# Kernel optimization log

Hardware: AMD Instinct MI355X
Metric: run time of the kernel (lower is better)

## Reference

```python
import jax, jax.numpy as jnp
import numpy as np

GRID = 14
N_HEADS = 12
TOP_K = 32


def _valid_indices(grid):
    """Replicates create_locality_mask: cls row/col always valid; patch pairs
    valid iff Chebyshev distance on the grid <= 2 (includes diagonal)."""
    n = grid * grid + 1
    mask = np.zeros((n, n), dtype=bool)
    mask[0, :] = True
    mask[:, 0] = True
    idx = np.arange(grid * grid)
    r, c = idx // grid, idx % grid
    cheb = np.maximum(np.abs(r[:, None] - r[None, :]), np.abs(c[:, None] - c[None, :]))
    mask[1:, 1:] = cheb <= 2
    i_idx, j_idx = np.nonzero(mask)
    return jnp.asarray(i_idx, dtype=jnp.int32), jnp.asarray(j_idx, dtype=jnp.int32)

I_IDX, J_IDX = _valid_indices(GRID)  # nv = 4489 valid (query, key) pairs


def setup_inputs() -> dict:
    key = jax.random.key(0)
    ks = jax.random.split(key, 6)
    B, L, D = 32, GRID * GRID + 1, 768
    s = 0.02
    return {
        "x": jax.random.normal(ks[0], (B, L, D), jnp.float32),
        "W_q": jax.random.normal(ks[1], (D, D), jnp.float32) * s,
        "b_q": jnp.zeros((D,), jnp.float32),
        "W_k": jax.random.normal(ks[2], (D, D), jnp.float32) * s,
        "b_k": jnp.zeros((D,), jnp.float32),
        "W_v": jax.random.normal(ks[3], (D, D), jnp.float32) * s,
        "b_v": jnp.zeros((D,), jnp.float32),
        "W_o": jax.random.normal(ks[4], (D, D), jnp.float32) * s,
        "b_o": jnp.zeros((D,), jnp.float32),
        "log_sigma": jnp.zeros((), jnp.float32),  # sigma = 1.0
    }


def reference(x, W_q, b_q, W_k, b_k, W_v, b_v, W_o, b_o, log_sigma):
    B, L, D = x.shape
    H, dk = N_HEADS, D // N_HEADS

    def proj(W, b):
        y = jnp.einsum('bld,de->ble', x, W) + b
        return y.reshape(B, L, H, dk).transpose(0, 2, 1, 3)  # [B,H,L,dk]

    Q, K, V = proj(W_q, b_q), proj(W_k, b_k), proj(W_v, b_v)

    sigma_sq = jnp.exp(2.0 * log_sigma)
    # gather valid (i,j) pairs; nv pairs from the locality mask
    q_valid = Q[:, :, I_IDX, :]                       # [B,H,nv,dk]
    k_valid = K[:, :, J_IDX, :]                       # [B,H,nv,dk]
    dist_sq = jnp.sum((q_valid - k_valid) ** 2, axis=-1)  # [B,H,nv]
    scores_valid = (-0.5 / sigma_sq) * dist_sq

    neg_inf = jnp.array(-jnp.inf, x.dtype)
    scores = jnp.full((B, H, L, L), neg_inf, dtype=x.dtype)
    scores = scores.at[:, :, I_IDX, J_IDX].set(scores_valid)

    k_top = min(TOP_K, L)
    _, top_idx = jax.lax.top_k(scores, k_top)          # [B,H,L,k]
    bb = jnp.arange(B)[:, None, None, None]
    hh = jnp.arange(H)[None, :, None, None]
    nn = jnp.arange(L)[None, None, :, None]
    topk_mask = jnp.zeros((B, H, L, L), bool).at[bb, hh, nn, top_idx].set(True)

    final_mask = jnp.isfinite(scores) & topk_mask
    scores = jnp.where(final_mask, scores, neg_inf)
    weights = jax.nn.softmax(scores, axis=-1)          # [B,H,L,L]
    attention_mask = (weights > 1e-6).astype(x.dtype)

    consensus = jnp.einsum('bhij,bhjd->bhid', weights, V)
    consensus = consensus.transpose(0, 2, 1, 3).reshape(B, L, D)
    out = jnp.einsum('bld,de->ble', consensus, W_o) + b_o
    return out, weights, attention_mask
```

## Files before the change

kernel.cpp:

```cpp
#include <hip/hip_runtime.h>
#include <hip/hip_bf16.h>
#include <math.h>

#define GRIDN 14
#define L 197
#define H 12
#define DK 64
#define D 768
#define B 32
#define BL (B*L)
#define TOPK 32
#define NBH (B*H)
#define NROW (NBH*L)
#define QKV_ELEMS ((size_t)NROW*DK)

typedef __attribute__((ext_vector_type(8))) short short8;
typedef __attribute__((ext_vector_type(4))) float floatx4;

__device__ __forceinline__ void load_lds16(void* lds, const void* g) {
    __builtin_amdgcn_global_load_lds(
        (const __attribute__((address_space(1))) unsigned int*)g,
        (__attribute__((address_space(3))) unsigned int*)lds, 16, 0, 0);
}

__global__ __launch_bounds__(256)
void prep(const float* __restrict__ x,
          const float* __restrict__ Wq, const float* __restrict__ Wk,
          const float* __restrict__ Wv, const float* __restrict__ Wo,
          __hip_bfloat16* __restrict__ xh, __hip_bfloat16* __restrict__ xl,
          __hip_bfloat16* __restrict__ WqTh, __hip_bfloat16* __restrict__ WqTl,
          __hip_bfloat16* __restrict__ WkTh, __hip_bfloat16* __restrict__ WkTl,
          __hip_bfloat16* __restrict__ WvT,  __hip_bfloat16* __restrict__ WoT)
{
    const int z = blockIdx.z;
    if (z == 4) {
        int lin = (blockIdx.y * 24 + blockIdx.x) * 256 + threadIdx.x;
        for (int i = lin; i < BL * D / 4; i += 24 * 24 * 256) {
            float4 v = ((const float4*)x)[i];
            union { __hip_bfloat16 b[4]; short4 s; } hh, ll;
            float f[4] = {v.x, v.y, v.z, v.w};
            #pragma unroll
            for (int j = 0; j < 4; ++j) {
                __hip_bfloat16 h = __float2bfloat16(f[j]);
                hh.b[j] = h;
                ll.b[j] = __float2bfloat16(f[j] - __bfloat162float(h));
            }
            ((short4*)xh)[i] = hh.s;
            ((short4*)xl)[i] = ll.s;
        }
        return;
    }
    __shared__ float tile[32][33];
    const float* src = (z == 0) ? Wq : (z == 1) ? Wk : (z == 2) ? Wv : Wo;
    __hip_bfloat16* dh = (z == 0) ? WqTh : (z == 1) ? WkTh : (z == 2) ? WvT : WoT;
    __hip_bfloat16* dl = (z == 0) ? WqTl : (z == 1) ? WkTl : nullptr;
    const int k0 = blockIdx.y * 32, n0 = blockIdx.x * 32;
    const int tx = threadIdx.x & 31, ty = threadIdx.x >> 5;

    for (int r = ty; r < 32; r += 8)
        tile[r][tx] = src[(size_t)(k0 + r) * D + n0 + tx];
    __syncthreads();
    for (int r = ty; r < 32; r += 8) {
        float v = tile[tx][r];
        __hip_bfloat16 h = __float2bfloat16(v);
        dh[(size_t)(n0 + r) * D + k0 + tx] = h;
        if (dl) dl[(size_t)(n0 + r) * D + k0 + tx] =
            __float2bfloat16(v - __bfloat162float(h));
    }
}

__global__ __launch_bounds__(256)
void gemm_qkv(const __hip_bfloat16* __restrict__ xh, const __hip_bfloat16* __restrict__ xl,
              const __hip_bfloat16* __restrict__ Wqh, const __hip_bfloat16* __restrict__ Wql,
              const __hip_bfloat16* __restrict__ Wkh, const __hip_bfloat16* __restrict__ Wkl,
              const __hip_bfloat16* __restrict__ Wvh,
              const float* __restrict__ bq, const float* __restrict__ bk,
              const float* __restrict__ bv,
              float* __restrict__ Qb, float* __restrict__ Kb, float* __restrict__ Vb)
{
    __shared__ __attribute__((aligned(16))) __hip_bfloat16 Ash[128 * 32];
    __shared__ __attribute__((aligned(16))) __hip_bfloat16 Bsh[128 * 32];
    __shared__ __attribute__((aligned(16))) __hip_bfloat16 Asl[128 * 32];
    __shared__ __attribute__((aligned(16))) __hip_bfloat16 Bsl[128 * 32];

    const int grp = blockIdx.y / 6, nt = blockIdx.y % 6;
    const __hip_bfloat16 *Bth, *Btl; const float* bias; float* C;
    if (grp == 0)      { Bth = Wqh; Btl = Wql; bias = bq; C = Qb; }
    else if (grp == 1) { Bth = Wkh; Btl = Wkl; bias = bk; C = Kb; }
    else               { Bth = Wvh; Btl = nullptr; bias = bv; C = Vb; }
    const bool split = (grp < 2);

    const int tid = threadIdx.x;
    const int wave = tid >> 6, lane = tid & 63;
    const int quad = lane >> 4, l16 = lane & 15;
    const int m0 = blockIdx.x * 128, n0 = nt * 128;
    const int wm = (wave & 1) * 64, wn = (wave >> 1) * 64;

    floatx4 acc[4][4] = {};

    int s_r[2], s_cs[2];
    #pragma unroll
    for (int u = 0; u < 2; ++u) {
        int idx = tid + u * 256;
        s_r[u] = idx >> 2; s_cs[u] = idx & 3;
    }

    for (int k0 = 0; k0 < D; k0 += 32) {
        #pragma unroll
        for (int u = 0; u < 2; ++u) {
            int r = s_r[u];
            int csrc = s_cs[u] ^ ((r >> 1) & 3);
            int gm = m0 + r; if (gm >= BL) gm = BL - 1;
            size_t aoff = (size_t)gm * D + k0 + csrc * 8;
            size_t boff = (size_t)(n0 + r) * D + k0 + csrc * 8;
            int lds_off = (wave * 64 + u * 256) * 16;
            load_lds16((char*)Ash + lds_off, xh + aoff);
            load_lds16((char*)Bsh + lds_off, Bth + boff);
            if (split) {
                load_lds16((char*)Asl + lds_off, xl + aoff);
                load_lds16((char*)Bsl + lds_off, Btl + boff);
            }
        }
        __syncthreads();

        short8 ah[4], bh[4];
        #pragma unroll
        for (int a = 0; a < 4; ++a) {
            int r = wm + a * 16 + l16;
            int slot = (r << 2) + (quad ^ ((r >> 1) & 3));
            ah[a] = *(const short8*)((const char*)Ash + (slot << 4));
        }
        #pragma unroll
        for (int b2 = 0; b2 < 4; ++b2) {
            int r = wn + b2 * 16 + l16;
            int slot = (r << 2) + (quad ^ ((r >> 1) & 3));
            bh[b2] = *(const short8*)((const char*)Bsh + (slot << 4));
        }
        if (split) {
            short8 al[4], bl[4];
            #pragma unroll
            for (int a = 0; a < 4; ++a) {
                int r = wm + a * 16 + l16;
                int slot = (r << 2) + (quad ^ ((r >> 1) & 3));
                al[a] = *(const short8*)((const char*)Asl + (slot << 4));
            }
            #pragma unroll
            for (int b2 = 0; b2 < 4; ++b2) {
                int r = wn + b2 * 16 + l16;
                int slot = (r << 2) + (quad ^ ((r >> 1) & 3));
                bl[b2] = *(const short8*)((const char*)Bsl + (slot << 4));
            }
            #pragma unroll
            for (int a = 0; a < 4; ++a)
                #pragma unroll
                for (int b2 = 0; b2 < 4; ++b2) {
                    acc[a][b2] = __builtin_amdgcn_mfma_f32_16x16x32_bf16(
                        al[a], bh[b2], acc[a][b2], 0, 0, 0);
                    acc[a][b2] = __builtin_amdgcn_mfma_f32_16x16x32_bf16(
                        ah[a], bl[b2], acc[a][b2], 0, 0, 0);
                }
        }
        #pragma unroll
        for (int a = 0; a < 4; ++a)
            #pragma unroll
            for (int b2 = 0; b2 < 4; ++b2)
                acc[a][b2] = __builtin_amdgcn_mfma_f32_16x16x32_bf16(
                    ah[a], bh[b2], acc[a][b2], 0, 0, 0);
        __syncthreads();
    }

    #pragma unroll
    for (int b2 = 0; b2 < 4; ++b2) {
        int n = n0 + wn + b2 * 16 + l16;
        float bvv = bias[n];
        int hh = n >> 6, dd = n & 63;
        #pragma unroll
        for (int a = 0; a < 4; ++a) {
            #pragma unroll
            for (int r = 0; r < 4; ++r) {
                int m = m0 + wm + a * 16 + quad * 4 + r;
                if (m < BL) {
                    int bb = m / L, ll = m % L;
                    C[((((size_t)bb * H + hh) * L + ll) << 6) + dd] =
                        acc[a][b2][r] + bvv;
                }
            }
        }
    }
}

__global__ __launch_bounds__(256)
void gemm_o(const __hip_bfloat16* __restrict__ A,
            const __hip_bfloat16* __restrict__ Bt,
            const float* __restrict__ bias, float* __restrict__ C)
{
    __shared__ __attribute__((aligned(16))) __hip_bfloat16 As[128 * 32];
    __shared__ __attribute__((aligned(16))) __hip_bfloat16 Bts[128 * 32];

    const int tid = threadIdx.x;
    const int wave = tid >> 6, lane = tid & 63;
    const int quad = lane >> 4, l16 = lane & 15;
    const int m0 = blockIdx.x * 128, n0 = blockIdx.y * 128;
    const int wm = (wave & 1) * 64, wn = (wave >> 1) * 64;

    floatx4 acc[4][4] = {};

    int s_r[2], s_cs[2];
    #pragma unroll
    for (int u = 0; u < 2; ++u) {
        int idx = tid + u * 256;
        s_r[u] = idx >> 2; s_cs[u] = idx & 3;
    }

    for (int k0 = 0; k0 < D; k0 += 32) {
        #pragma unroll
        for (int u = 0; u < 2; ++u) {
            int r = s_r[u];
            int csrc = s_cs[u] ^ ((r >> 1) & 3);
            int gm = m0 + r; if (gm >= BL) gm = BL - 1;
            int lds_off = (wave * 64 + u * 256) * 16;
            load_lds16((char*)As + lds_off, A + (size_t)gm * D + k0 + csrc * 8);
            load_lds16((char*)Bts + lds_off, Bt + (size_t)(n0 + r) * D + k0 + csrc * 8);
        }
        __syncthreads();

        short8 af[4], bf[4];
        #pragma unroll
        for (int a = 0; a < 4; ++a) {
            int r = wm + a * 16 + l16;
            int slot = (r << 2) + (quad ^ ((r >> 1) & 3));
            af[a] = *(const short8*)((const char*)As + (slot << 4));
        }
        #pragma unroll
        for (int b2 = 0; b2 < 4; ++b2) {
            int r = wn + b2 * 16 + l16;
            int slot = (r << 2) + (quad ^ ((r >> 1) & 3));
            bf[b2] = *(const short8*)((const char*)Bts + (slot << 4));
        }
        #pragma unroll
        for (int a = 0; a < 4; ++a)
            #pragma unroll
            for (int b2 = 0; b2 < 4; ++b2)
                acc[a][b2] = __builtin_amdgcn_mfma_f32_16x16x32_bf16(
                    af[a], bf[b2], acc[a][b2], 0, 0, 0);
        __syncthreads();
    }

    #pragma unroll
    for (int b2 = 0; b2 < 4; ++b2) {
        int n = n0 + wn + b2 * 16 + l16;
        float bvv = bias[n];
        #pragma unroll
        for (int a = 0; a < 4; ++a) {
            #pragma unroll
            for (int r = 0; r < 4; ++r) {
                int m = m0 + wm + a * 16 + quad * 4 + r;
                if (m < BL) C[(size_t)m * D + n] = acc[a][b2][r] + bvv;
            }
        }
    }
}

__global__ __launch_bounds__(512)
void attn_fused(const float* __restrict__ Q, const float* __restrict__ Kg,
                const float* __restrict__ Vg, const float* __restrict__ logsig,
                float* __restrict__ wout, float* __restrict__ mout,
                __hip_bfloat16* __restrict__ cons)
{
    __shared__ float qbuf[8][64];
    __shared__ float clsbuf[L];
    __shared__ float wjW[99][32];
    __shared__ unsigned char wjJ[99][32];
    __shared__ unsigned int winA[L];
    __shared__ unsigned int winB[L];
    __shared__ unsigned char joff[76];

    const int bh = blockIdx.x;
    const int yb = blockIdx.y;
    const int b = bh / H, h = bh % H;
    const int tid = threadIdx.x, wave = tid >> 6, lane = tid & 63;
    const int base_i = yb * 99;
    const int half = lane & 1;

    if (tid >= 1 && tid < L) {
        int r = (tid - 1) / GRIDN, c = (tid - 1) % GRIDN;
        int r0 = r - 2 < 0 ? 0 : r - 2, r1 = r + 2 > 13 ? 13 : r + 2;
        int c0 = c - 2 < 0 ? 0 : c - 2, c1 = c + 2 > 13 ? 13 : c + 2;
        int Wd = c1 - c0 + 1, Hh = r1 - r0 + 1;
        winA[tid] = (unsigned)r0 | ((unsigned)c0 << 8) |
                    ((unsigned)Wd << 16) | ((unsigned)Hh << 24);
        winB[tid] = (unsigned)(Hh * Wd + 1) |
                    ((unsigned)(1 + r0 * GRIDN + c0) << 8);
    }
    if (tid == 0) { winA[0] = 0; winB[0] = 0; }
    if (tid < 75) {
        int w = tid / 25 + 3, tm = tid % 25;
        joff[tid] = (unsigned char)((tm / w) * GRIDN + tm % w);
    }

    int pr4[4], pc4[4];
    #pragma unroll
    for (int k = 0; k < 4; ++k) {
        int p = lane + (k << 6);
        if (p >= 1 && p < L) { pr4[k] = (p - 1) / GRIDN; pc4[k] = (p - 1) % GRIDN; }
        else                 { pr4[k] = 255; pc4[k] = 255; }
    }

    const float* Kp = Kg + (size_t)bh * L * DK;
    const float* Vp = Vg + (size_t)bh * L * DK;
    __syncthreads();

    const float coef = -0.5f * expf(-2.0f * logsig[0]);
    const int starts0[9] = {0, 9, 22, 35, 48, 61, 74, 87, 99};
    const int starts1[9] = {99, 112, 124, 136, 148, 161, 173, 185, 197};
    const int i_begin = yb ? starts1[wave] : starts0[wave];
    const int i_end   = yb ? starts1[wave + 1] : starts0[wave + 1];

    float qreg = (i_begin < i_end)
               ? Q[((size_t)bh * L + i_begin) * 64 + lane] : 0.f;

    for (int i = i_begin; i < i_end; ++i) {
        const int rowid = bh * L + i;
        const size_t wb = (size_t)rowid * L;
        const int local = i - base_i;

        qbuf[wave][lane] = qreg;
        if (i + 1 < i_end)
            qreg = Q[((size_t)rowid + 1) * 64 + lane];

        if (i == 0) {
            const float4* qp = (const float4*)&qbuf[wave][half << 5];
            for (int p = 0; p < 7; ++p) {
                int t = (p << 5) + (lane >> 1);
                bool valid = t < L;
                float s = 0.f;
                if (valid) {
                    const float4* kp = (const float4*)&Kp[(size_t)t * DK + (half << 5)];
                    #pragma unroll
                    for (int d4 = 0; d4 < 8; ++d4) {
                        float4 qv = qp[d4], kv = kp[d4];
                        float dx = qv.x - kv.x, dy = qv.y - kv.y;
                        float dz = qv.z - kv.z, dw = qv.w - kv.w;
                        s += dx * dx + dy * dy + dz * dz + dw * dw;
                    }
                }
                s += __shfl_xor(s, 1);
                if (valid && !half) clsbuf[t] = coef * s;
            }
            float orig[4], cur[4]; int selb = 0;
            #pragma unroll
            for (int k = 0; k < 4; ++k) {
                int t = lane + (k << 6);
                float v = (t < L) ? clsbuf[t] : -INFINITY;
                orig[k] = v; cur[k] = v;
            }
            float gmax = -INFINITY;
            for (int it = 0; it < TOPK; ++it) {
                float bv = cur[0]; int bt = lane;
                #pragma unroll
                for (int k = 1; k < 4; ++k)
                    if (cur[k] > bv) { bv = cur[k]; bt = lane + (k << 6); }
                #pragma unroll
                for (int off = 32; off; off >>= 1) {
                    float ov = __shfl_xor(bv, off);
                    int   ot = __shfl_xor(bt, off);
                    if (ov > bv || (ov == bv && ot < bt)) { bv = ov; bt = ot; }
                }
                if (it == 0) gmax = bv;
                if ((bt & 63) == lane) { cur[bt >> 6] = -INFINITY; selb |= 1 << (bt >> 6); }
            }
            float zl = 0.f; float wk[4];
            #pragma unroll
            for (int k = 0; k < 4; ++k) {
                wk[k] = ((selb >> k) & 1) ? expf(orig[k] - gmax) : 0.f;
                zl += wk[k];
            }
            #pragma unroll
            for (int off = 32; off; off >>= 1) zl += __shfl_xor(zl, off);

            #pragma unroll
            for (int k = 0; k < 4; ++k) {
                int p = lane + (k << 6);
                if (p < L) {
                    float wv = wk[k] / zl;
                    wout[wb + p] = wv;
                    mout[wb + p] = (wv > 1e-6f) ? 1.f : 0.f;
                }
            }
            int slot = 0;
            #pragma unroll
            for (int k = 0; k < 4; ++k) {
                bool sel = (selb >> k) & 1;
                unsigned long long mk = __ballot(sel);
                if (sel) {
                    int tt = slot + (int)__popcll(mk & ((1ull << lane) - 1ull));
                    wjW[0][tt] = wk[k] / zl;
                    wjJ[0][tt] = (unsigned char)(lane + (k << 6));
                }
                slot += (int)__popcll(mk);
            }
        } else {
            const unsigned wa = winA[i], wbp = winB[i];
            const int r0 = wa & 255, c0 = (wa >> 8) & 255;
            const int Wd2 = (wa >> 16) & 255, Hh = wa >> 24;
            const int n = wbp & 255, jbase = wbp >> 8;

            int t = lane >> 1;
            bool valid = t < n;
            float s = 0.f; int j = 0;
            if (valid) {
                if (t > 0) j = jbase + joff[(Wd2 - 3) * 25 + (t - 1)];
                const float4* kp = (const float4*)&Kp[(size_t)j * DK + (half << 5)];
                const float4* qp = (const float4*)&qbuf[wave][half << 5];
                #pragma unroll
                for (int d4 = 0; d4 < 8; ++d4) {
                    float4 qv = qp[d4], kv = kp[d4];
                    float dx = qv.x - kv.x, dy = qv.y - kv.y;
                    float dz = qv.z - kv.z, dw = qv.w - kv.w;
                    s += dx * dx + dy * dy + dz * dz + dw * dw;
                }
            }
            s += __shfl_xor(s, 1);
            float sc = valid ? coef * s : -INFINITY;

            float mx = sc;
            #pragma unroll
            for (int off = 32; off; off >>= 1) mx = fmaxf(mx, __shfl_xor(mx, off));
            float e = valid ? expf(sc - mx) : 0.f;
            float es = half ? 0.f : e;
            #pragma unroll
            for (int off = 32; off; off >>= 1) es += __shfl_xor(es, off);
            float wv = e / es;

            if (!half) {
                float wcv = valid ? wv : 0.f;
                wjW[local][t] = wcv;
                wjJ[local][t] = (unsigned char)(valid ? j : 0);
            }
            #pragma unroll
            for (int k = 0; k < 4; ++k) {
                int p = lane + (k << 6);
                if (p < L) {
                    float wd = 0.f;
                    if (p == 0) wd = wjW[local][0];
                    else {
                        unsigned du = (unsigned)(pr4[k] - r0);
                        unsigned dv = (unsigned)(pc4[k] - c0);
                        if (du < (unsigned)Hh && dv < (unsigned)Wd2)
                            wd = wjW[local][1 + du * Wd2 + dv];
                    }
                    wout[wb + p] = wd;
                    mout[wb + p] = (wd > 1e-6f) ? 1.f : 0.f;
                }
            }
        }
    }
    __syncthreads();

    const int cstarts0[9] = {0, 13, 26, 38, 50, 62, 74, 87, 99};
    const int c_begin = yb ? starts1[wave] : cstarts0[wave];
    const int c_end   = yb ? starts1[wave + 1] : cstarts0[wave + 1];

    for (int i = c_begin; i < c_end; ++i) {
        const int local = i - base_i;
        float acc = 0.f;
        #pragma unroll
        for (int t = 0; t < 32; ++t) {
            float w = wjW[local][t];
            int j = wjJ[local][t];
            acc += w * Vp[(size_t)j * DK + lane];
        }
        cons[((size_t)b * L + i) * D + h * 64 + lane] = __float2bfloat16(acc);
    }
}

extern "C" void kernel_launch(void* const* d_in, const int* in_sizes, int n_in,
                              void* d_out, int out_size, void* d_ws, size_t ws_size,
                              hipStream_t stream)
{
    const float* x   = (const float*)d_in[0];
    const float* Wq  = (const float*)d_in[1];
    const float* bq  = (const float*)d_in[2];
    const float* Wk  = (const float*)d_in[3];
    const float* bk  = (const float*)d_in[4];
    const float* Wv  = (const float*)d_in[5];
    const float* bv  = (const float*)d_in[6];
    const float* Wo  = (const float*)d_in[7];
    const float* bo  = (const float*)d_in[8];
    const float* lsg = (const float*)d_in[9];

    float* out  = (float*)d_out;
    float* wout = out + QKV_ELEMS;
    float* mout = wout + (size_t)B * H * L * L;

    float* Qb  = (float*)d_ws;
    float* Kb  = Qb + QKV_ELEMS;
    float* Vb  = Kb + QKV_ELEMS;
    __hip_bfloat16* xh = (__hip_bfloat16*)(Vb + QKV_ELEMS);
    __hip_bfloat16* xl = xh + (size_t)BL * D;
    __hip_bfloat16* WqTh = xl + (size_t)BL * D;
    __hip_bfloat16* WqTl = WqTh + (size_t)D * D;
    __hip_bfloat16* WkTh = WqTl + (size_t)D * D;
    __hip_bfloat16* WkTl = WkTh + (size_t)D * D;
    __hip_bfloat16* WvT  = WkTl + (size_t)D * D;
    __hip_bfloat16* WoT  = WvT  + (size_t)D * D;
    __hip_bfloat16* consb = xh;

    prep<<<dim3(24, 24, 5), 256, 0, stream>>>(
        x, Wq, Wk, Wv, Wo, xh, xl, WqTh, WqTl, WkTh, WkTl, WvT, WoT);

    gemm_qkv<<<dim3(50, 18), 256, 0, stream>>>(
        xh, xl, WqTh, WqTl, WkTh, WkTl, WvT, bq, bk, bv, Qb, Kb, Vb);

    attn_fused<<<dim3(NBH, 2), 512, 0, stream>>>(
        Qb, Kb, Vb, lsg, wout, mout, consb);

    gemm_o<<<dim3(50, 6), 256, 0, stream>>>(consb, WoT, bo, out);
}
```

Measured before the change: 398.4 us.

## Stage K and V row windows in LDS for attention distance and consensus

Each attention block first copies the 127 K rows its half of the queries can touch (the cls row plus an offset window) into padded shared memory and computes distances from LDS rather than global memory. After the score phase, the same buffer is refilled with V rows for the weighted-sum step; the cls query row still reads V from global memory. Per-row window parameters are now computed arithmetically instead of through LDS lookup tables, and launch bounds request higher occupancy. This trades roughly 34KB of LDS and two extra barriers per block for fewer scattered global loads, which may reduce resident blocks per CU.

```diff
diff --git a/kernel.cpp b/kernel.cpp
--- a/kernel.cpp
+++ b/kernel.cpp
@@ -13,6 +13,8 @@
 #define NBH (B*H)
 #define NROW (NBH*L)
 #define QKV_ELEMS ((size_t)NROW*DK)
+#define KSTR 68
+#define KROWS 127
 
 typedef __attribute__((ext_vector_type(8))) short short8;
 typedef __attribute__((ext_vector_type(4))) float floatx4;
@@ -261,18 +263,17 @@
     }
 }
 
-__global__ __launch_bounds__(512)
+__global__ __launch_bounds__(512, 8)
 void attn_fused(const float* __restrict__ Q, const float* __restrict__ Kg,
                 const float* __restrict__ Vg, const float* __restrict__ logsig,
                 float* __restrict__ wout, float* __restrict__ mout,
                 __hip_bfloat16* __restrict__ cons)
 {
+    __shared__ __attribute__((aligned(16))) float KV[KROWS * KSTR];
     __shared__ float qbuf[8][64];
     __shared__ float clsbuf[L];
     __shared__ float wjW[99][32];
     __shared__ unsigned char wjJ[99][32];
-    __shared__ unsigned int winA[L];
-    __shared__ unsigned int winB[L];
     __shared__ unsigned char joff[76];
 
     const int bh = blockIdx.x;
@@ -281,18 +282,8 @@
     const int tid = threadIdx.x, wave = tid >> 6, lane = tid & 63;
     const int base_i = yb * 99;
     const int half = lane & 1;
-
-    if (tid >= 1 && tid < L) {
-        int r = (tid - 1) / GRIDN, c = (tid - 1) % GRIDN;
-        int r0 = r - 2 < 0 ? 0 : r - 2, r1 = r + 2 > 13 ? 13 : r + 2;
-        int c0 = c - 2 < 0 ? 0 : c - 2, c1 = c + 2 > 13 ? 13 : c + 2;
-        int Wd = c1 - c0 + 1, Hh = r1 - r0 + 1;
-        winA[tid] = (unsigned)r0 | ((unsigned)c0 << 8) |
-                    ((unsigned)Wd << 16) | ((unsigned)Hh << 24);
-        winB[tid] = (unsigned)(Hh * Wd + 1) |
-                    ((unsigned)(1 + r0 * GRIDN + c0) << 8);
-    }
-    if (tid == 0) { winA[0] = 0; winB[0] = 0; }
+    const int joffs = yb ? 70 : 0;
+
     if (tid < 75) {
         int w = tid / 25 + 3, tm = tid % 25;
         joff[tid] = (unsigned char)((tm / w) * GRIDN + tm % w);
@@ -307,7 +298,11 @@
     }
 
     const float* Kp = Kg + (size_t)bh * L * DK;
-    const float* Vp = Vg + (size_t)bh * L * DK;
+    for (int idx = tid; idx < KROWS * 16; idx += 512) {
+        int r = idx >> 4, c4 = idx & 15;
+        int g = r ? r + joffs : 0;
+        *(float4*)&KV[r * KSTR + c4 * 4] = *(const float4*)&Kp[g * 64 + c4 * 4];
+    }
     __syncthreads();
 
     const float coef = -0.5f * expf(-2.0f * logsig[0]);
@@ -400,17 +395,24 @@
                 slot += (int)__popcll(mk);
             }
         } else {
-            const unsigned wa = winA[i], wbp = winB[i];
-            const int r0 = wa & 255, c0 = (wa >> 8) & 255;
-            const int Wd2 = (wa >> 16) & 255, Hh = wa >> 24;
-            const int n = wbp & 255, jbase = wbp >> 8;
+            const int pi = i - 1;
+            const int pr = (pi * 9363) >> 17;
+            const int pc = pi - pr * GRIDN;
+            const int r0 = pr - 2 < 0 ? 0 : pr - 2;
+            const int r1 = pr + 2 > 13 ? 13 : pr + 2;
+            const int c0 = pc - 2 < 0 ? 0 : pc - 2;
+            const int c1 = pc + 2 > 13 ? 13 : pc + 2;
+            const int Wd2 = c1 - c0 + 1, Hh = r1 - r0 + 1;
+            const int n = Hh * Wd2 + 1;
+            const int jbase = 1 + r0 * GRIDN + c0;
 
             int t = lane >> 1;
             bool valid = t < n;
             float s = 0.f; int j = 0;
             if (valid) {
                 if (t > 0) j = jbase + joff[(Wd2 - 3) * 25 + (t - 1)];
-                const float4* kp = (const float4*)&Kp[(size_t)j * DK + (half << 5)];
+                int js = j ? j - joffs : 0;
+                const float4* kp = (const float4*)&KV[js * KSTR + (half << 5)];
                 const float4* qp = (const float4*)&qbuf[wave][half << 5];
                 #pragma unroll
                 for (int d4 = 0; d4 < 8; ++d4) {
@@ -457,6 +459,14 @@
     }
     __syncthreads();
 
+    const float* Vp = Vg + (size_t)bh * L * DK;
+    for (int idx = tid; idx < KROWS * 16; idx += 512) {
+        int r = idx >> 4, c4 = idx & 15;
+        int g = r ? r + joffs : 0;
+        *(float4*)&KV[r * KSTR + c4 * 4] = *(const float4*)&Vp[g * 64 + c4 * 4];
+    }
+    __syncthreads();
+
     const int cstarts0[9] = {0, 13, 26, 38, 50, 62, 74, 87, 99};
     const int c_begin = yb ? starts1[wave] : cstarts0[wave];
     const int c_end   = yb ? starts1[wave + 1] : cstarts0[wave + 1];
@@ -464,11 +474,21 @@
     for (int i = c_begin; i < c_end; ++i) {
         const int local = i - base_i;
         float acc = 0.f;
-        #pragma unroll
-        for (int t = 0; t < 32; ++t) {
-            float w = wjW[local][t];
-            int j = wjJ[local][t];
-            acc += w * Vp[(size_t)j * DK + lane];
+        if (i == 0) {
+            #pragma unroll
+            for (int t = 0; t < 32; ++t) {
+                float w = wjW[0][t];
+                int j = wjJ[0][t];
+                acc += w * Vp[(size_t)j * DK + lane];
+            }
+        } else {
+            #pragma unroll
+            for (int t = 0; t < 32; ++t) {
+                float w = wjW[local][t];
+                int j = wjJ[local][t];
+                int js = j ? j - joffs : 0;
+                acc += w * KV[js * KSTR + lane];
+            }
         }
         cons[((size_t)b * L + i) * D + h * 64 + lane] = __float2bfloat16(acc);
     }
```

Result: faster. 388.4 us (-2.5%).
